# Performance work log

Hardware: AMD Instinct MI355X
Metric: run time of the kernel (lower is better)

## Reference

```python
import jax, jax.numpy as jnp
import numpy as np

B, T, D = 32, 512, 1024   # batch, seq_len, input_dim
H, L, O = 1024, 4, 1024   # hidden_dim, num_layers, output_dim


def setup_inputs() -> dict:
    key = jax.random.key(0)
    ks = jax.random.split(key, 8)
    s_in = 1.0 / np.sqrt(D)
    s_h = 1.0 / np.sqrt(H)
    # Weights stored as [in, out]; y = x @ W + b (equivalent to torch Linear with W.T)
    return {
        "x":     jax.random.normal(ks[0], (B, T, D), dtype=jnp.float32),
        "W_in":  jax.random.uniform(ks[1], (L, D, H), minval=-s_in, maxval=s_in, dtype=jnp.float32),
        "b_in":  jax.random.uniform(ks[2], (L, H),    minval=-s_in, maxval=s_in, dtype=jnp.float32),
        "W_h":   jax.random.uniform(ks[3], (L, H, H), minval=-s_h,  maxval=s_h,  dtype=jnp.float32),
        "b_h":   jax.random.uniform(ks[4], (L, H),    minval=-s_h,  maxval=s_h,  dtype=jnp.float32),
        "tau":   jnp.ones((L, H), dtype=jnp.float32),
        "W_out": jax.random.uniform(ks[5], (H, O),    minval=-s_h,  maxval=s_h,  dtype=jnp.float32),
        "b_out": jax.random.uniform(ks[6], (O,),      minval=-s_h,  maxval=s_h,  dtype=jnp.float32),
    }


def reference(x, W_in, b_in, W_h, b_h, tau, W_out, b_out):
    n_layers = W_in.shape[0]

    def step(h, x_t):
        # h: [L, B, H]; x_t: [B, D]
        xt = x_t
        new_h = []
        for i in range(n_layers):
            dx = jnp.tanh(xt @ W_in[i] + b_in[i] + h[i] @ W_h[i] + b_h[i])
            hi = h[i] + (dx - h[i]) / tau[i]
            new_h.append(hi)
            xt = hi
        return jnp.stack(new_h), None

    h0 = jnp.zeros((n_layers, x.shape[0], W_h.shape[-1]), dtype=x.dtype)
    hT, _ = jax.lax.scan(step, h0, jnp.swapaxes(x, 0, 1))  # scan over time axis
    return hT[-1] @ W_out + b_out  # [B, O]
```

## Files before the change

kernel.cpp:

```cpp
#include <hip/hip_runtime.h>
#include <math.h>

#define B_ 32
#define T_ 512
#define D_ 1024
#define H_ 1024
#define L_ 4
#define RPD 17
#define PACK_PER_BLK 32768

typedef unsigned long long u64;

__device__ __forceinline__ float4 load_state4(const float* p) {
    u64 a = __hip_atomic_load((const u64*)p,       __ATOMIC_RELAXED, __HIP_MEMORY_SCOPE_AGENT);
    u64 b = __hip_atomic_load((const u64*)(p + 2), __ATOMIC_RELAXED, __HIP_MEMORY_SCOPE_AGENT);
    float4 v;
    v.x = __uint_as_float((unsigned)(a & 0xffffffffu));
    v.y = __uint_as_float((unsigned)(a >> 32));
    v.z = __uint_as_float((unsigned)(b & 0xffffffffu));
    v.w = __uint_as_float((unsigned)(b >> 32));
    return v;
}

__device__ __forceinline__ void waitCount(const unsigned int* p, unsigned int target) {
    int c = 0;
    while (__hip_atomic_load(p, __ATOMIC_RELAXED, __HIP_MEMORY_SCOPE_AGENT) < target) {
        __builtin_amdgcn_s_sleep(16);
        if (++c > 20000) return;
    }
}

__global__ __launch_bounds__(512) void lnn_repack(
    const float* __restrict__ W_in, const float* __restrict__ W_h,
    float* __restrict__ Wpack)
{
    const int bid   = blockIdx.x;
    const int layer = bid >> 6;
    const int jbase = (bid & 63) << 4;
    const float* Win_l = W_in + (size_t)layer * D_ * H_;
    const float* Wh_l  = W_h  + (size_t)layer * H_ * H_;
    float* dst = Wpack + (size_t)bid * PACK_PER_BLK;
#pragma unroll 1
    for (int i = 0; i < 16; ++i) {
        const int f  = (i << 9) + threadIdx.x;
        const int d  = f << 2;
        const int jj = d >> 11;
        const int k  = d & 2047;
        const float* s = (k < 1024) ? &Win_l[(size_t)k * H_ + jbase + jj]
                                    : &Wh_l[(size_t)(k - 1024) * H_ + jbase + jj];
        float4 v;
        v.x = s[0];
        v.y = s[(size_t)H_];
        v.z = s[(size_t)2 * H_];
        v.w = s[(size_t)3 * H_];
        *(float4*)&dst[d] = v;
    }
}

#define REDUCE_PHASE(P)                                                         \
    do {                                                                        \
        __syncthreads();                                                        \
        _Pragma("unroll")                                                       \
        for (int q = 0; q < 8; ++q) {                                           \
            red[tid * RPD + (q << 1)]     = acc[((P) << 3) + q].x;              \
            red[tid * RPD + (q << 1) + 1] = acc[((P) << 3) + q].y;              \
        }                                                                       \
        __syncthreads();                                                        \
        if (tid < 128) {                                                        \
            const int bo   = tid >> 4;                                          \
            const int bh   = ((P) << 3) + bo;                                   \
            const int js   = (tid & 15) >> 1;                                   \
            const int comp = tid & 1;                                           \
            float s = 0.f;                                                      \
            _Pragma("unroll")                                                   \
            for (int ks = 0; ks < 64; ++ks)                                     \
                s += red[((ks << 3) + js) * RPD + (bo << 1) + comp];            \
            const float dx   = tanhf(s + bias);                                 \
            const float hold = __hip_atomic_load(&hrow[(size_t)bh * H_ + jr],   \
                                __ATOMIC_RELAXED, __HIP_MEMORY_SCOPE_AGENT);    \
            const float hn   = hold + (dx - hold) / tv;                         \
            __hip_atomic_store(&wl[(size_t)bh * H_ + jr], hn,                   \
                               __ATOMIC_RELAXED, __HIP_MEMORY_SCOPE_AGENT);     \
        }                                                                       \
    } while (0)

template<bool PACKED>
__global__ __launch_bounds__(512, 2) void lnn_persist(
    const float* __restrict__ x,
    const float* __restrict__ W_in,
    const float* __restrict__ b_in,
    const float* __restrict__ W_h,
    const float* __restrict__ b_h,
    const float* __restrict__ tau,
    const float* __restrict__ Wpack,
    float* __restrict__ buf0,
    float* __restrict__ buf1,
    unsigned int* __restrict__ done)
{
    const int tid   = threadIdx.x;
    const int layer = blockIdx.x >> 6;
    const int jbase = (blockIdx.x & 63) << 4;
    const int jp    = tid & 7;
    const int kslot = tid >> 3;
    const int kb    = kslot << 2;

    __shared__ __align__(16) float smem[16384];
    float (*xs)[32][256] = (float(*)[32][256])smem;
    float* red = smem;

    const float* Wl_in = W_in + (size_t)layer * D_ * H_;
    const float* Wl_h  = W_h  + (size_t)layer * H_ * H_;
    const float* wbaseA = Wpack + (size_t)blockIdx.x * PACK_PER_BLK
                        + ((size_t)(jp << 1) << 11);
    const float* wbaseB = wbaseA + 2048;
    const int jgA = jbase + (jp << 1);

    const int   jr   = jbase + (tid & 15);
    const float bias = b_in[layer * H_ + jr] + b_h[layer * H_ + jr];
    const float tv   = tau[layer * H_ + jr];

    const int srow = tid >> 6;
    const int scol = (tid & 63) << 2;

    for (int t = 0; t < T_; ++t) {
        if (tid == 0) {
            if (layer > 0)             waitCount(&done[(layer - 1) * T_ + t],     64u);
            if (t >= 1)                waitCount(&done[layer * T_ + (t - 1)],     64u);
            if (layer < 3 && t >= 2)   waitCount(&done[(layer + 1) * T_ + (t - 2)], 64u);
        }
        __syncthreads();

        const int par = (t + layer) & 1;
        const float* rb   = par ? buf0 : buf1;
        float*       wb   = par ? buf1 : buf0;
        const float* hrow = rb + (size_t)layer * B_ * H_;
        float*       wl   = wb + (size_t)layer * B_ * H_;

        const float* xsrc; size_t xstr;
        if (layer == 0) { xsrc = x + (size_t)t * D_;                  xstr = (size_t)T_ * D_; }
        else            { xsrc = rb + (size_t)(layer - 1) * B_ * H_;  xstr = H_; }

        float2 acc[32];
#pragma unroll
        for (int i = 0; i < 32; ++i) acc[i] = make_float2(0.f, 0.f);

        {
            const bool at0 = (layer != 0);
#pragma unroll
            for (int q = 0; q < 4; ++q) {
                const int r = srow + (q << 3);
                const float* sp = &xsrc[(size_t)r * xstr + scol];
                float4 v = at0 ? load_state4(sp) : *(const float4*)sp;
                *(float4*)&xs[0][r][scol] = v;
            }
        }
        __syncthreads();

#pragma unroll 1
        for (int tile = 0; tile < 8; ++tile) {
            const int cur = tile & 1;

            float4 wA, wB;
            if constexpr (PACKED) {
                wA = *(const float4*)&wbaseA[(tile << 8) + kb];
                wB = *(const float4*)&wbaseB[(tile << 8) + kb];
            } else {
                const int kof = (tile & 3) << 8;
                const float* wp = ((tile < 4) ? Wl_in : Wl_h)
                                + (size_t)(kof + kb) * H_ + jgA;
                wA.x = wp[0];            wB.x = wp[1];
                wA.y = wp[(size_t)H_];   wB.y = wp[(size_t)H_ + 1];
                wA.z = wp[2*(size_t)H_]; wB.z = wp[2*(size_t)H_ + 1];
                wA.w = wp[3*(size_t)H_]; wB.w = wp[3*(size_t)H_ + 1];
            }

            float4 stg[4];
            if (tile < 7) {
                const int    nt   = tile + 1;
                const float* nsrc = (nt < 4) ? xsrc : hrow;
                const size_t nstr = (nt < 4) ? xstr : (size_t)H_;
                const int    nkof = (nt & 3) << 8;
                const bool   nat  = (nt >= 4) || (layer != 0);
#pragma unroll
                for (int q = 0; q < 4; ++q) {
                    const int r = srow + (q << 3);
                    const float* sp = &nsrc[(size_t)r * nstr + nkof + scol];
                    stg[q] = nat ? load_state4(sp) : *(const float4*)sp;
                }
            }

#pragma unroll
            for (int b = 0; b < 32; ++b) {
                const float4 a = *(const float4*)&xs[cur][b][kb];
                acc[b].x += a.x * wA.x + a.y * wA.y + a.z * wA.z + a.w * wA.w;
                acc[b].y += a.x * wB.x + a.y * wB.y + a.z * wB.z + a.w * wB.w;
            }

            if (tile < 7) {
#pragma unroll
                for (int q = 0; q < 4; ++q)
                    *(float4*)&xs[cur ^ 1][srow + (q << 3)][scol] = stg[q];
            }
            __syncthreads();
        }

        REDUCE_PHASE(0); REDUCE_PHASE(1); REDUCE_PHASE(2); REDUCE_PHASE(3);

        __syncthreads();
        if (tid == 0)
            __hip_atomic_fetch_add(&done[layer * T_ + t], 1u,
                                   __ATOMIC_RELEASE, __HIP_MEMORY_SCOPE_AGENT);
    }
}

__global__ __launch_bounds__(256) void lnn_out(
    const float* __restrict__ H3,
    const float* __restrict__ W_out,
    const float* __restrict__ b_out,
    float* __restrict__ out)
{
    const int gid = blockIdx.x * 256 + threadIdx.x;
    const int jj  = gid & 1023;
    const int b2  = gid >> 10;
    float acc0 = b_out[jj];
    float acc1 = b_out[jj];
    for (int k = 0; k < H_; ++k) {
        const float w = W_out[k * H_ + jj];
        acc0 += H3[b2 * H_ + k]        * w;
        acc1 += H3[(b2 + 16) * H_ + k] * w;
    }
    out[b2 * H_ + jj]        = acc0;
    out[(b2 + 16) * H_ + jj] = acc1;
}

extern "C" void kernel_launch(void* const* d_in, const int* in_sizes, int n_in,
                              void* d_out, int out_size, void* d_ws, size_t ws_size,
                              hipStream_t stream) {
    const float* x     = (const float*)d_in[0];
    const float* W_in  = (const float*)d_in[1];
    const float* b_in  = (const float*)d_in[2];
    const float* W_h   = (const float*)d_in[3];
    const float* b_h   = (const float*)d_in[4];
    const float* tau   = (const float*)d_in[5];
    const float* W_out = (const float*)d_in[6];
    const float* b_out = (const float*)d_in[7];

    const size_t stateElems = (size_t)L_ * B_ * H_;
    const size_t packElems  = (size_t)256 * PACK_PER_BLK;
    const size_t cntDwords  = (size_t)L_ * T_;
    const size_t needPacked = (packElems + 2 * stateElems) * sizeof(float)
                            + cntDwords * sizeof(unsigned int);
    const bool packed = (ws_size >= needPacked);

    float* Wpack = (float*)d_ws;
    float* buf0  = packed ? (Wpack + packElems) : (float*)d_ws;
    float* buf1  = buf0 + stateElems;
    unsigned int* done = (unsigned int*)(buf1 + stateElems);

    (void)hipMemsetAsync(buf0, 0,
                         2 * stateElems * sizeof(float) + cntDwords * sizeof(unsigned int),
                         stream);

    if (packed) {
        lnn_repack<<<256, 512, 0, stream>>>(W_in, W_h, Wpack);
        lnn_persist<true><<<256, 512, 0, stream>>>(x, W_in, b_in, W_h, b_h, tau,
                                                   Wpack, buf0, buf1, done);
    } else {
        lnn_persist<false><<<256, 512, 0, stream>>>(x, W_in, b_in, W_h, b_h, tau,
                                                    Wpack, buf0, buf1, done);
    }

    const float* H3 = buf0 + 3 * (B_ * H_);
    lnn_out<<<64, 256, 0, stream>>>(H3, W_out, b_out, (float*)d_out);
}
```

Before: 13.31 ms.

## Reorder tiles to start recurrent matmul before waiting on previous layer

Measured after the change: 14.42 ms. 8.4% more time.

```diff
diff --git a/kernel.cpp b/kernel.cpp
--- a/kernel.cpp
+++ b/kernel.cpp
@@ -23,10 +23,13 @@
 }
 
 __device__ __forceinline__ void waitCount(const unsigned int* p, unsigned int target) {
+    for (int c = 0; c < 256; ++c)
+        if (__hip_atomic_load(p, __ATOMIC_RELAXED, __HIP_MEMORY_SCOPE_AGENT) >= target)
+            return;
     int c = 0;
     while (__hip_atomic_load(p, __ATOMIC_RELAXED, __HIP_MEMORY_SCOPE_AGENT) < target) {
-        __builtin_amdgcn_s_sleep(16);
-        if (++c > 20000) return;
+        __builtin_amdgcn_s_sleep(2);
+        if (++c > 200000) return;
     }
 }
 
@@ -123,11 +126,8 @@
     const int scol = (tid & 63) << 2;
 
     for (int t = 0; t < T_; ++t) {
-        if (tid == 0) {
-            if (layer > 0)             waitCount(&done[(layer - 1) * T_ + t],     64u);
-            if (t >= 1)                waitCount(&done[layer * T_ + (t - 1)],     64u);
-            if (layer < 3 && t >= 2)   waitCount(&done[(layer + 1) * T_ + (t - 2)], 64u);
-        }
+        if (tid == 0 && t >= 1)
+            waitCount(&done[layer * T_ + (t - 1)], 64u);
         __syncthreads();
 
         const int par = (t + layer) & 1;
@@ -145,20 +145,19 @@
         for (int i = 0; i < 32; ++i) acc[i] = make_float2(0.f, 0.f);
 
         {
-            const bool at0 = (layer != 0);
 #pragma unroll
             for (int q = 0; q < 4; ++q) {
                 const int r = srow + (q << 3);
-                const float* sp = &xsrc[(size_t)r * xstr + scol];
-                float4 v = at0 ? load_state4(sp) : *(const float4*)sp;
-                *(float4*)&xs[0][r][scol] = v;
+                const float* sp = &hrow[(size_t)r * H_ + scol];
+                *(float4*)&xs[0][r][scol] = load_state4(sp);
             }
         }
         __syncthreads();
 
 #pragma unroll 1
-        for (int tile = 0; tile < 8; ++tile) {
-            const int cur = tile & 1;
+        for (int ti = 0; ti < 8; ++ti) {
+            const int tile = (ti + 4) & 7;
+            const int cur  = ti & 1;
 
             float4 wA, wB;
             if constexpr (PACKED) {
@@ -174,9 +173,15 @@
                 wA.w = wp[3*(size_t)H_]; wB.w = wp[3*(size_t)H_ + 1];
             }
 
+            if (ti == 3 && layer > 0) {
+                if (tid == 0)
+                    waitCount(&done[(layer - 1) * T_ + t], 64u);
+                __syncthreads();
+            }
+
             float4 stg[4];
-            if (tile < 7) {
-                const int    nt   = tile + 1;
+            if (ti < 7) {
+                const int    nt   = (ti + 5) & 7;
                 const float* nsrc = (nt < 4) ? xsrc : hrow;
                 const size_t nstr = (nt < 4) ? xstr : (size_t)H_;
                 const int    nkof = (nt & 3) << 8;
@@ -196,13 +201,16 @@
                 acc[b].y += a.x * wB.x + a.y * wB.y + a.z * wB.z + a.w * wB.w;
             }
 
-            if (tile < 7) {
+            if (ti < 7) {
 #pragma unroll
                 for (int q = 0; q < 4; ++q)
                     *(float4*)&xs[cur ^ 1][srow + (q << 3)][scol] = stg[q];
             }
             __syncthreads();
         }
+
+        if (tid == 0 && layer < 3 && t >= 2)
+            waitCount(&done[(layer + 1) * T_ + (t - 2)], 64u);
 
         REDUCE_PHASE(0); REDUCE_PHASE(1); REDUCE_PHASE(2); REDUCE_PHASE(3);
 
```

## Retile per-thread work to 16 rows x 4 columns and tighten spin-wait polling

Applied to the files above, without the earlier changes.

Measured after the change: 15.78 ms. 1.19x slower.

```diff
diff --git a/kernel.cpp b/kernel.cpp
--- a/kernel.cpp
+++ b/kernel.cpp
@@ -6,7 +6,7 @@
 #define D_ 1024
 #define H_ 1024
 #define L_ 4
-#define RPD 17
+#define RPW 40
 #define PACK_PER_BLK 32768
 
 typedef unsigned long long u64;
@@ -23,10 +23,13 @@
 }
 
 __device__ __forceinline__ void waitCount(const unsigned int* p, unsigned int target) {
+    for (int c = 0; c < 256; ++c)
+        if (__hip_atomic_load(p, __ATOMIC_RELAXED, __HIP_MEMORY_SCOPE_AGENT) >= target)
+            return;
     int c = 0;
     while (__hip_atomic_load(p, __ATOMIC_RELAXED, __HIP_MEMORY_SCOPE_AGENT) < target) {
-        __builtin_amdgcn_s_sleep(16);
-        if (++c > 20000) return;
+        __builtin_amdgcn_s_sleep(2);
+        if (++c > 200000) return;
     }
 }
 
@@ -59,27 +62,31 @@
 
 #define REDUCE_PHASE(P)                                                         \
     do {                                                                        \
+        constexpr int bhp  = (P) >> 1;                                          \
+        constexpr int rloc = ((P) & 1) << 3;                                    \
         __syncthreads();                                                        \
-        _Pragma("unroll")                                                       \
-        for (int q = 0; q < 8; ++q) {                                           \
-            red[tid * RPD + (q << 1)]     = acc[((P) << 3) + q].x;              \
-            red[tid * RPD + (q << 1) + 1] = acc[((P) << 3) + q].y;              \
+        if (bh == bhp) {                                                        \
+            const int wrow = (kslot << 2) + jq;                                 \
+            _Pragma("unroll")                                                   \
+            for (int q = 0; q < 8; ++q)                                         \
+                *(float4*)&red[wrow * RPW + (q << 2)] = acc[rloc + q];          \
         }                                                                       \
         __syncthreads();                                                        \
         if (tid < 128) {                                                        \
-            const int bo   = tid >> 4;                                          \
-            const int bh   = ((P) << 3) + bo;                                   \
-            const int js   = (tid & 15) >> 1;                                   \
-            const int comp = tid & 1;                                           \
+            const int bo   = tid >> 4;                    \
+            const int bhat = ((P) << 3) + bo;           \
+            const int jhat = tid & 15;                                          \
+            const int sj   = jhat >> 2;                          \
+            const int cc   = jhat & 3;                     \
             float s = 0.f;                                                      \
             _Pragma("unroll")                                                   \
             for (int ks = 0; ks < 64; ++ks)                                     \
-                s += red[((ks << 3) + js) * RPD + (bo << 1) + comp];            \
+                s += red[((ks << 2) + sj) * RPW + (bo << 2) + cc];              \
             const float dx   = tanhf(s + bias);                                 \
-            const float hold = __hip_atomic_load(&hrow[(size_t)bh * H_ + jr],   \
+            const float hold = __hip_atomic_load(&hrow[(size_t)bhat * H_ + jr], \
                                 __ATOMIC_RELAXED, __HIP_MEMORY_SCOPE_AGENT);    \
             const float hn   = hold + (dx - hold) / tv;                         \
-            __hip_atomic_store(&wl[(size_t)bh * H_ + jr], hn,                   \
+            __hip_atomic_store(&wl[(size_t)bhat * H_ + jr], hn,                 \
                                __ATOMIC_RELAXED, __HIP_MEMORY_SCOPE_AGENT);     \
         }                                                                       \
     } while (0)
@@ -100,7 +107,8 @@
     const int tid   = threadIdx.x;
     const int layer = blockIdx.x >> 6;
     const int jbase = (blockIdx.x & 63) << 4;
-    const int jp    = tid & 7;
+    const int jq    = tid & 3;
+    const int bh    = (tid >> 2) & 1;
     const int kslot = tid >> 3;
     const int kb    = kslot << 2;
 
@@ -110,10 +118,12 @@
 
     const float* Wl_in = W_in + (size_t)layer * D_ * H_;
     const float* Wl_h  = W_h  + (size_t)layer * H_ * H_;
-    const float* wbaseA = Wpack + (size_t)blockIdx.x * PACK_PER_BLK
-                        + ((size_t)(jp << 1) << 11);
-    const float* wbaseB = wbaseA + 2048;
-    const int jgA = jbase + (jp << 1);
+    const float* wb0 = Wpack + (size_t)blockIdx.x * PACK_PER_BLK
+                     + ((size_t)((jq << 2) + 0) << 11);
+    const float* wb1 = wb0 + 2048;
+    const float* wb2 = wb0 + 4096;
+    const float* wb3 = wb0 + 6144;
+    const int jgA = jbase + (jq << 2);
 
     const int   jr   = jbase + (tid & 15);
     const float bias = b_in[layer * H_ + jr] + b_h[layer * H_ + jr];
@@ -124,8 +134,8 @@
 
     for (int t = 0; t < T_; ++t) {
         if (tid == 0) {
-            if (layer > 0)             waitCount(&done[(layer - 1) * T_ + t],     64u);
-            if (t >= 1)                waitCount(&done[layer * T_ + (t - 1)],     64u);
+            if (layer > 0)             waitCount(&done[(layer - 1) * T_ + t],       64u);
+            if (t >= 1)                waitCount(&done[layer * T_ + (t - 1)],       64u);
             if (layer < 3 && t >= 2)   waitCount(&done[(layer + 1) * T_ + (t - 2)], 64u);
         }
         __syncthreads();
@@ -140,9 +150,9 @@
         if (layer == 0) { xsrc = x + (size_t)t * D_;                  xstr = (size_t)T_ * D_; }
         else            { xsrc = rb + (size_t)(layer - 1) * B_ * H_;  xstr = H_; }
 
-        float2 acc[32];
-#pragma unroll
-        for (int i = 0; i < 32; ++i) acc[i] = make_float2(0.f, 0.f);
+        float4 acc[16];
+#pragma unroll
+        for (int i = 0; i < 16; ++i) acc[i] = make_float4(0.f, 0.f, 0.f, 0.f);
 
         {
             const bool at0 = (layer != 0);
@@ -160,18 +170,24 @@
         for (int tile = 0; tile < 8; ++tile) {
             const int cur = tile & 1;
 
-            float4 wA, wB;
+            float4 w0, w1, w2, w3;
             if constexpr (PACKED) {
-                wA = *(const float4*)&wbaseA[(tile << 8) + kb];
-                wB = *(const float4*)&wbaseB[(tile << 8) + kb];
+                w0 = *(const float4*)&wb0[(tile << 8) + kb];
+                w1 = *(const float4*)&wb1[(tile << 8) + kb];
+                w2 = *(const float4*)&wb2[(tile << 8) + kb];
+                w3 = *(const float4*)&wb3[(tile << 8) + kb];
             } else {
                 const int kof = (tile & 3) << 8;
                 const float* wp = ((tile < 4) ? Wl_in : Wl_h)
                                 + (size_t)(kof + kb) * H_ + jgA;
-                wA.x = wp[0];            wB.x = wp[1];
-                wA.y = wp[(size_t)H_];   wB.y = wp[(size_t)H_ + 1];
-                wA.z = wp[2*(size_t)H_]; wB.z = wp[2*(size_t)H_ + 1];
-                wA.w = wp[3*(size_t)H_]; wB.w = wp[3*(size_t)H_ + 1];
+                w0.x = wp[0];              w1.x = wp[1];
+                w0.y = wp[(size_t)H_];     w1.y = wp[(size_t)H_ + 1];
+                w0.z = wp[2*(size_t)H_];   w1.z = wp[2*(size_t)H_ + 1];
+                w0.w = wp[3*(size_t)H_];   w1.w = wp[3*(size_t)H_ + 1];
+                w2.x = wp[2];              w3.x = wp[3];
+                w2.y = wp[(size_t)H_ + 2]; w3.y = wp[(size_t)H_ + 3];
+                w2.z = wp[2*(size_t)H_+2]; w3.z = wp[2*(size_t)H_ + 3];
+                w2.w = wp[3*(size_t)H_+2]; w3.w = wp[3*(size_t)H_ + 3];
             }
 
             float4 stg[4];
@@ -190,10 +206,13 @@
             }
 
 #pragma unroll
-            for (int b = 0; b < 32; ++b) {
-                const float4 a = *(const float4*)&xs[cur][b][kb];
-                acc[b].x += a.x * wA.x + a.y * wA.y + a.z * wA.z + a.w * wA.w;
-                acc[b].y += a.x * wB.x + a.y * wB.y + a.z * wB.z + a.w * wB.w;
+            for (int r = 0; r < 16; ++r) {
+                const int row = (bh << 4) + r;
+                const float4 a = *(const float4*)&xs[cur][row][kb];
+                acc[r].x += a.x * w0.x + a.y * w0.y + a.z * w0.z + a.w * w0.w;
+                acc[r].y += a.x * w1.x + a.y * w1.y + a.z * w1.z + a.w * w1.w;
+                acc[r].z += a.x * w2.x + a.y * w2.y + a.z * w2.z + a.w * w2.w;
+                acc[r].w += a.x * w3.x + a.y * w3.y + a.z * w3.z + a.w * w3.w;
             }
 
             if (tile < 7) {
```
